# Kernel tuning notes

Measured on AMD Instinct MI355X. Metric: run time of the kernel, lower is better.

## Reference

```python
import jax, jax.numpy as jnp
import numpy as np

ROUTING_ITERS = 3


def squash(v):
    # v: [..., D]; l2norm over last dim
    l2 = jnp.linalg.norm(v, axis=-1, keepdims=True)
    unit = v / l2
    factor = (l2 * l2) / (1.0 + l2 * l2)
    return unit * factor


def setup_inputs() -> dict:
    key = jax.random.key(0)
    k1, k2 = jax.random.split(key)
    B, N_in, D_in = 256, 1152, 8
    N_out, D_out = 10, 16
    x = jax.random.normal(k1, (B, N_in, D_in), dtype=jnp.float32)
    W = jax.random.normal(k2, (N_in, N_out, D_out, D_in), dtype=jnp.float32)
    return {"x": x, "W": W}


def reference(x, W):
    # x: [B, N_in, D_in], W: [N_in, N_out, D_out, D_in]
    # u_hat[b,i,o,:] = W[i,o] @ x[b,i]
    u_hat = jnp.einsum('iodk,bik->biod', W, x)  # [B, N_in, N_out, D_out]
    N_in, N_out = W.shape[0], W.shape[1]
    b_logits = jnp.zeros((N_in, N_out), dtype=x.dtype)
    s = None
    for r in range(ROUTING_ITERS + 1):
        c = jax.nn.softmax(b_logits, axis=-1)            # [N_in, N_out]
        s = jnp.einsum('io,biod->bod', c, u_hat)          # [B, N_out, D_out]
        s = squash(s)
        if r < ROUTING_ITERS:
            # agreement summed over batch (matches original .sum(dim=0))
            b_logits = b_logits + jnp.einsum('biod,bod->io', u_hat, s)
    return s
```

## Files before the change

### kernel.cpp

```cpp
#include <hip/hip_runtime.h>
#include <math.h>

typedef __attribute__((ext_vector_type(8))) short bf16x8;
typedef __attribute__((ext_vector_type(4))) float f32x4;
typedef unsigned short u16;
typedef unsigned int u32;

#define NI    1152
#define DI    8
#define NO    10
#define DOUT  16
#define F     160
#define KTOT  9216
#define KS    288
#define SK    72

#define OFF_W2F 0
#define OFF_XFH 1474560
#define OFF_XFL 2654208
#define OFF_XTH 3833856
#define OFF_XTL 5013504
#define OFF_SFH 6193152
#define OFF_SFL 6213632
#define OFF_P   6234112
#define OFF_BA  9183232
#define OFF_BB  9194752
#define OFF_TP  9206272

union U8 { u16 u[8]; uint4 v; };

__device__ inline u16 bf16hi(float x) {
    u32 u = __float_as_uint(x);
    return (u16)((u + 0x7FFFu + ((u >> 16) & 1u)) >> 16);
}
__device__ inline float bf2f(u16 h) { return __uint_as_float(((u32)h) << 16); }

__global__ void prep(const float* __restrict__ x, const float* __restrict__ W,
                     float* __restrict__ W2f,
                     u16* __restrict__ xfh, u16* __restrict__ xfl,
                     u16* __restrict__ xth, u16* __restrict__ xtl,
                     float* __restrict__ blogA) {
    int u = blockIdx.x * 256 + threadIdx.x;
    if (u < 184320) {
        if (u < NI * NO) blogA[u] = 0.f;
        int ul = u & 63, tmp = u >> 6;
        int ks = tmp % KS, o = tmp / KS;
        int i = ks * 4 + (ul >> 4), d = ul & 15;
        const float* wp = W + ((size_t)(i * NO + o) * DOUT + d) * DI;
        float4 a = ((const float4*)wp)[0], b = ((const float4*)wp)[1];
        float* dst = W2f + (size_t)tmp * 512 + ul * 8;
        ((float4*)dst)[0] = a; ((float4*)dst)[1] = b;
    } else if (u < 479232) {
        int q = u - 184320;
        int ul = q & 63, tmp = q >> 6;
        int ks = tmp % KS, mt = tmp / KS;
        const float* xp = x + (size_t)(mt * 16 + (ul & 15)) * KTOT + ks * 32 + (ul >> 4) * 8;
        float4 a = ((const float4*)xp)[0], b = ((const float4*)xp)[1];
        float v[8] = {a.x, a.y, a.z, a.w, b.x, b.y, b.z, b.w};
        U8 ph, pl;
#pragma unroll
        for (int j = 0; j < 8; j++) {
            u16 h = bf16hi(v[j]);
            ph.u[j] = h; pl.u[j] = bf16hi(v[j] - bf2f(h));
        }
        *(uint4*)(xfh + (size_t)tmp * 512 + ul * 8) = ph.v;
        *(uint4*)(xfl + (size_t)tmp * 512 + ul * 8) = pl.v;
    } else if (u < 774144) {
        int q = u - 479232;
        int ul = q & 63, tmp = q >> 6;
        int ks8 = tmp & 7, ns = tmp >> 3;
        U8 ph, pl;
#pragma unroll
        for (int j = 0; j < 8; j++) {
            float v = x[(size_t)(ks8 * 32 + (ul >> 4) * 8 + j) * KTOT + ns * 16 + (ul & 15)];
            u16 h = bf16hi(v);
            ph.u[j] = h; pl.u[j] = bf16hi(v - bf2f(h));
        }
        *(uint4*)(xth + (size_t)tmp * 512 + ul * 8) = ph.v;
        *(uint4*)(xtl + (size_t)tmp * 512 + ul * 8) = pl.v;
    }
}

__global__ __launch_bounds__(256) void s_round(const u16* __restrict__ xfh,
                                               const u16* __restrict__ xfl,
                                               const float* __restrict__ W2f,
                                               const float* __restrict__ tpart,
                                               const float* __restrict__ blogIn,
                                               float* __restrict__ blogOut,
                                               float* __restrict__ P, int isR0) {
    __shared__ __attribute__((aligned(16))) u16 cwhS[10240];
    __shared__ __attribute__((aligned(16))) u16 cwlS[10240];
    __shared__ float ts[16][NO];
    __shared__ float cls[16][NO];

    const int t = threadIdx.x, l = t & 63, w = t >> 6;
    const int bid = blockIdx.x;
    const int sk  = bid % SK;
    const int fh  = (bid / SK) & 1;
    const int btg = bid / (2 * SK);

    if (isR0) {
        if (t < 160) cls[t / NO][t % NO] = 0.1f;
    } else {
        if (t < 160) {
            int il = t / NO, o = t % NO;
            int ig = sk * 16 + il;
            float a = tpart[(size_t)ig * NO + o] +
                      tpart[(size_t)(NI + ig) * NO + o] +
                      tpart[(size_t)(2 * NI + ig) * NO + o] +
                      tpart[(size_t)(3 * NI + ig) * NO + o];
            float bnew = blogIn[ig * NO + o] + a;
            blogOut[ig * NO + o] = bnew;
            ts[il][o] = bnew;
        }
        __syncthreads();
        if (t < 16) {
            float m = -3.402823466e+38f;
#pragma unroll
            for (int o = 0; o < NO; o++) m = fmaxf(m, ts[t][o]);
            float e[NO];
            float sum = 0.f;
#pragma unroll
            for (int o = 0; o < NO; o++) { e[o] = expf(ts[t][o] - m); sum += e[o]; }
            float inv = 1.f / sum;
#pragma unroll
            for (int o = 0; o < NO; o++) cls[t][o] = e[o] * inv;
        }
    }
    __syncthreads();

#pragma unroll
    for (int p = 0; p < 5; p++) {
        int vid  = p * 256 + t;
        int frag = vid >> 6;
        int ll   = vid & 63;
        int n = frag >> 2, kk = frag & 3;
        int ks = sk * 4 + kk;
        float cv = cls[kk * 4 + (ll >> 4)][fh * 5 + n];
        size_t base = ((size_t)((fh * 5 + n) * KS + ks)) * 512 + ll * 8;
        float4 a = ((const float4*)(W2f + base))[0];
        float4 b = ((const float4*)(W2f + base))[1];
        float v[8] = {a.x, a.y, a.z, a.w, b.x, b.y, b.z, b.w};
        U8 ph, pl;
#pragma unroll
        for (int j = 0; j < 8; j++) {
            float pv = cv * v[j];
            u16 h = bf16hi(pv);
            ph.u[j] = h; pl.u[j] = bf16hi(pv - bf2f(h));
        }
        *(uint4*)(cwhS + frag * 512 + ll * 8) = ph.v;
        *(uint4*)(cwlS + frag * 512 + ll * 8) = pl.v;
    }
    __syncthreads();

    const int bt = btg * 4 + w;
    f32x4 z = {0.f, 0.f, 0.f, 0.f};
    f32x4 acc[5];
#pragma unroll
    for (int n = 0; n < 5; n++) acc[n] = z;

#pragma unroll
    for (int kk = 0; kk < 4; kk++) {
        int ks = sk * 4 + kk;
        size_t ai = ((size_t)(bt * KS + ks)) * 512 + l * 8;
        bf16x8 ah = *(const bf16x8*)(xfh + ai);
        bf16x8 al = *(const bf16x8*)(xfl + ai);
#pragma unroll
        for (int n = 0; n < 5; n++) {
            bf16x8 bh = *(const bf16x8*)(cwhS + (n * 4 + kk) * 512 + l * 8);
            bf16x8 bl = *(const bf16x8*)(cwlS + (n * 4 + kk) * 512 + l * 8);
            acc[n] = __builtin_amdgcn_mfma_f32_16x16x32_bf16(ah, bh, acc[n], 0, 0, 0);
            acc[n] = __builtin_amdgcn_mfma_f32_16x16x32_bf16(ah, bl, acc[n], 0, 0, 0);
            acc[n] = __builtin_amdgcn_mfma_f32_16x16x32_bf16(al, bh, acc[n], 0, 0, 0);
        }
    }
    const int c0 = l & 15, rg = l >> 4;
    float* Pp = P + (size_t)sk * 40960 + (size_t)(bt * 16 + rg * 4) * F + fh * 80 + c0;
#pragma unroll
    for (int n = 0; n < 5; n++)
#pragma unroll
        for (int rr = 0; rr < 4; rr++)
            Pp[(size_t)rr * F + n * 16] = acc[n][rr];
}

__global__ void rs(const float* __restrict__ P, float* __restrict__ sout,
                   u16* __restrict__ sfh, u16* __restrict__ sfl) {
    int idx = blockIdx.x * 256 + threadIdx.x;
    float sum = 0.f;
#pragma unroll 8
    for (int sk2 = 0; sk2 < SK; sk2++) sum += P[(size_t)sk2 * 40960 + idx];
    float n2 = sum * sum;
#pragma unroll
    for (int off = 8; off > 0; off >>= 1) n2 += __shfl_xor(n2, off, 16);
    float l2v = sqrtf(n2);
    float scale = l2v / (1.f + n2);
    float sv = sum * scale;
    sout[idx] = sv;
    int b = idx / F, f = idx % F;
    size_t si = (size_t)((f >> 4) * 8 + (b >> 5)) * 512 +
                (size_t)(((b >> 3) & 3) * 16 + (f & 15)) * 8 + (b & 7);
    u16 h = bf16hi(sv);
    sfh[si] = h;
    sfl[si] = bf16hi(sv - bf2f(h));
}

__global__ __launch_bounds__(256) void c1(const u16* __restrict__ sfh,
                                          const u16* __restrict__ sfl,
                                          const u16* __restrict__ xth,
                                          const u16* __restrict__ xtl,
                                          const float* __restrict__ W,
                                          float* __restrict__ tpart) {
    __shared__ __attribute__((aligned(16))) float G[160 * 68];
    const int t = threadIdx.x, l = t & 63, w = t >> 6;
    const int nb = blockIdx.x >> 2, bq = blockIdx.x & 3;
    const int wm = w & 1, wn = w >> 1;

    f32x4 z = {0.f, 0.f, 0.f, 0.f};
    f32x4 acc[5][2];
#pragma unroll
    for (int m = 0; m < 5; m++)
#pragma unroll
        for (int n = 0; n < 2; n++) acc[m][n] = z;

#pragma unroll
    for (int ksl = 0; ksl < 2; ksl++) {
        int ksb = bq * 2 + ksl;
        bf16x8 ah[5], al[5];
#pragma unroll
        for (int m = 0; m < 5; m++) {
            size_t ai = ((size_t)((wm * 5 + m) * 8 + ksb)) * 512 + l * 8;
            ah[m] = *(const bf16x8*)(sfh + ai);
            al[m] = *(const bf16x8*)(sfl + ai);
        }
#pragma unroll
        for (int nl = 0; nl < 2; nl++) {
            size_t bi = ((size_t)((nb * 4 + wn * 2 + nl) * 8 + ksb)) * 512 + l * 8;
            bf16x8 bh = *(const bf16x8*)(xth + bi);
            bf16x8 blo = *(const bf16x8*)(xtl + bi);
#pragma unroll
            for (int m = 0; m < 5; m++) {
                acc[m][nl] = __builtin_amdgcn_mfma_f32_16x16x32_bf16(ah[m], bh, acc[m][nl], 0, 0, 0);
                acc[m][nl] = __builtin_amdgcn_mfma_f32_16x16x32_bf16(ah[m], blo, acc[m][nl], 0, 0, 0);
                acc[m][nl] = __builtin_amdgcn_mfma_f32_16x16x32_bf16(al[m], bh, acc[m][nl], 0, 0, 0);
            }
        }
    }
    const int c0 = l & 15, rg = l >> 4;
#pragma unroll
    for (int m = 0; m < 5; m++)
#pragma unroll
        for (int nl = 0; nl < 2; nl++)
#pragma unroll
            for (int rr = 0; rr < 4; rr++)
                G[(wm * 80 + m * 16 + rg * 4 + rr) * 68 + wn * 32 + nl * 16 + c0] = acc[m][nl][rr];
    __syncthreads();
    if (t < 160) {
        int i_l = t / 20, o = (t % 20) >> 1, dh = t & 1;
        int i_g = nb * 8 + i_l;
        const float* wp = W + (size_t)(i_g * NO + o) * 128 + dh * 64;
        float sum = 0.f;
#pragma unroll
        for (int d = 0; d < 8; d++) {
            const float* gp = &G[(o * 16 + dh * 8 + d) * 68 + i_l * 8];
            float4 g0 = ((const float4*)gp)[0], g1 = ((const float4*)gp)[1];
            float4 w0 = ((const float4*)(wp + d * 8))[0], w1 = ((const float4*)(wp + d * 8))[1];
            sum += g0.x * w0.x + g0.y * w0.y + g0.z * w0.z + g0.w * w0.w +
                   g1.x * w1.x + g1.y * w1.y + g1.z * w1.z + g1.w * w1.w;
        }
        sum += __shfl_xor(sum, 1);
        if (dh == 0) tpart[(size_t)(bq * NI + i_g) * NO + o] = sum;
    }
}

extern "C" void kernel_launch(void* const* d_in, const int* in_sizes, int n_in,
                              void* d_out, int out_size, void* d_ws, size_t ws_size,
                              hipStream_t stream) {
    const float* x = (const float*)d_in[0];
    const float* W = (const float*)d_in[1];
    float* out = (float*)d_out;
    float* ws  = (float*)d_ws;
    float* W2f = ws + OFF_W2F;
    u16* xfh = (u16*)(ws + OFF_XFH);
    u16* xfl = (u16*)(ws + OFF_XFL);
    u16* xth = (u16*)(ws + OFF_XTH);
    u16* xtl = (u16*)(ws + OFF_XTL);
    u16* sfh = (u16*)(ws + OFF_SFH);
    u16* sfl = (u16*)(ws + OFF_SFL);
    float* P   = ws + OFF_P;
    float* blA = ws + OFF_BA;
    float* blB = ws + OFF_BB;
    float* tp  = ws + OFF_TP;

    prep<<<3024, 256, 0, stream>>>(x, W, W2f, xfh, xfl, xth, xtl, blA);

    for (int r = 0; r < 4; r++) {
        const float* bIn = (r == 2) ? blB : blA;
        float* bOut      = (r == 2) ? blA : blB;
        s_round<<<576, 256, 0, stream>>>(xfh, xfl, W2f, tp, bIn, bOut, P, r == 0 ? 1 : 0);
        rs<<<160, 256, 0, stream>>>(P, out, sfh, sfl);
        if (r < 3)
            c1<<<576, 256, 0, stream>>>(sfh, sfl, xth, xtl, W, tp);
    }
}
```

Before: 100.1 us.

## Fuse routing s-round and squash reduction into one kernel per round

Replaces the split-K s_round kernel and the separate rs reduction with one sq_round kernel. Each 1024-thread block owns one 16-batch tile and one output capsule, and its 16 waves split K and reduce through shared memory before squashing. This removes the large partial-sum buffer P, its write and read traffic, and one launch per round. Routing logits now accumulate in place in c1 through taccum (+=), and each block recomputes softmax over all inputs, which replaces the logit ping-pong buffers. The cost is only 160 blocks instead of 576, plus much more repeated L2 reading of W2f and x across blocks.

```diff
diff --git a/kernel.cpp b/kernel.cpp
--- a/kernel.cpp
+++ b/kernel.cpp
@@ -13,7 +13,6 @@
 #define F     160
 #define KTOT  9216
 #define KS    288
-#define SK    72
 
 #define OFF_W2F 0
 #define OFF_XFH 1474560
@@ -22,12 +21,9 @@
 #define OFF_XTL 5013504
 #define OFF_SFH 6193152
 #define OFF_SFL 6213632
-#define OFF_P   6234112
-#define OFF_BA  9183232
-#define OFF_BB  9194752
-#define OFF_TP  9206272
-
-union U8 { u16 u[8]; uint4 v; };
+#define OFF_TP  6234112
+
+union U8 { u16 u[8]; uint4 v; bf16x8 b; };
 
 __device__ inline u16 bf16hi(float x) {
     u32 u = __float_as_uint(x);
@@ -39,10 +35,10 @@
                      float* __restrict__ W2f,
                      u16* __restrict__ xfh, u16* __restrict__ xfl,
                      u16* __restrict__ xth, u16* __restrict__ xtl,
-                     float* __restrict__ blogA) {
+                     float* __restrict__ taccum) {
     int u = blockIdx.x * 256 + threadIdx.x;
     if (u < 184320) {
-        if (u < NI * NO) blogA[u] = 0.f;
+        if (u < 4 * NI * NO) taccum[u] = 0.f;
         int ul = u & 63, tmp = u >> 6;
         int ks = tmp % KS, o = tmp / KS;
         int i = ks * 4 + (ul >> 4), d = ul & 15;
@@ -81,127 +77,88 @@
     }
 }
 
-__global__ __launch_bounds__(256) void s_round(const u16* __restrict__ xfh,
-                                               const u16* __restrict__ xfl,
-                                               const float* __restrict__ W2f,
-                                               const float* __restrict__ tpart,
-                                               const float* __restrict__ blogIn,
-                                               float* __restrict__ blogOut,
-                                               float* __restrict__ P, int isR0) {
-    __shared__ __attribute__((aligned(16))) u16 cwhS[10240];
-    __shared__ __attribute__((aligned(16))) u16 cwlS[10240];
-    __shared__ float ts[16][NO];
-    __shared__ float cls[16][NO];
+__global__ __launch_bounds__(1024) void sq_round(const u16* __restrict__ xfh,
+                                                 const u16* __restrict__ xfl,
+                                                 const float* __restrict__ W2f,
+                                                 const float* __restrict__ taccum,
+                                                 u16* __restrict__ sfh,
+                                                 u16* __restrict__ sfl,
+                                                 float* __restrict__ out, int r) {
+    __shared__ float cls[NI];
+    __shared__ __attribute__((aligned(16))) float Pl[16 * 256];
 
     const int t = threadIdx.x, l = t & 63, w = t >> 6;
-    const int bid = blockIdx.x;
-    const int sk  = bid % SK;
-    const int fh  = (bid / SK) & 1;
-    const int btg = bid / (2 * SK);
-
-    if (isR0) {
-        if (t < 160) cls[t / NO][t % NO] = 0.1f;
-    } else {
-        if (t < 160) {
-            int il = t / NO, o = t % NO;
-            int ig = sk * 16 + il;
-            float a = tpart[(size_t)ig * NO + o] +
-                      tpart[(size_t)(NI + ig) * NO + o] +
-                      tpart[(size_t)(2 * NI + ig) * NO + o] +
-                      tpart[(size_t)(3 * NI + ig) * NO + o];
-            float bnew = blogIn[ig * NO + o] + a;
-            blogOut[ig * NO + o] = bnew;
-            ts[il][o] = bnew;
-        }
-        __syncthreads();
-        if (t < 16) {
-            float m = -3.402823466e+38f;
-#pragma unroll
-            for (int o = 0; o < NO; o++) m = fmaxf(m, ts[t][o]);
-            float e[NO];
-            float sum = 0.f;
-#pragma unroll
-            for (int o = 0; o < NO; o++) { e[o] = expf(ts[t][o] - m); sum += e[o]; }
-            float inv = 1.f / sum;
-#pragma unroll
-            for (int o = 0; o < NO; o++) cls[t][o] = e[o] * inv;
-        }
+    const int btg = blockIdx.x;
+    const int o   = blockIdx.y;
+
+    for (int i = t; i < NI; i += 1024) {
+        float bv[NO];
+        float m = -3.402823466e+38f;
+#pragma unroll
+        for (int oo = 0; oo < NO; oo++) {
+            float a = taccum[i * NO + oo] + taccum[(NI + i) * NO + oo] +
+                      taccum[(2 * NI + i) * NO + oo] + taccum[(3 * NI + i) * NO + oo];
+            bv[oo] = a;
+            m = fmaxf(m, a);
+        }
+        float sum = 0.f;
+#pragma unroll
+        for (int oo = 0; oo < NO; oo++) { bv[oo] = expf(bv[oo] - m); sum += bv[oo]; }
+        cls[i] = bv[o] * (1.f / sum);
     }
     __syncthreads();
 
-#pragma unroll
-    for (int p = 0; p < 5; p++) {
-        int vid  = p * 256 + t;
-        int frag = vid >> 6;
-        int ll   = vid & 63;
-        int n = frag >> 2, kk = frag & 3;
-        int ks = sk * 4 + kk;
-        float cv = cls[kk * 4 + (ll >> 4)][fh * 5 + n];
-        size_t base = ((size_t)((fh * 5 + n) * KS + ks)) * 512 + ll * 8;
-        float4 a = ((const float4*)(W2f + base))[0];
-        float4 b = ((const float4*)(W2f + base))[1];
-        float v[8] = {a.x, a.y, a.z, a.w, b.x, b.y, b.z, b.w};
-        U8 ph, pl;
-#pragma unroll
-        for (int j = 0; j < 8; j++) {
-            float pv = cv * v[j];
-            u16 h = bf16hi(pv);
-            ph.u[j] = h; pl.u[j] = bf16hi(pv - bf2f(h));
-        }
-        *(uint4*)(cwhS + frag * 512 + ll * 8) = ph.v;
-        *(uint4*)(cwlS + frag * 512 + ll * 8) = pl.v;
-    }
-    __syncthreads();
-
-    const int bt = btg * 4 + w;
-    f32x4 z = {0.f, 0.f, 0.f, 0.f};
-    f32x4 acc[5];
-#pragma unroll
-    for (int n = 0; n < 5; n++) acc[n] = z;
-
-#pragma unroll
-    for (int kk = 0; kk < 4; kk++) {
-        int ks = sk * 4 + kk;
-        size_t ai = ((size_t)(bt * KS + ks)) * 512 + l * 8;
+    f32x4 acc = {0.f, 0.f, 0.f, 0.f};
+    const int ks0 = w * 18;
+#pragma unroll 3
+    for (int kk = 0; kk < 18; kk++) {
+        int ks = ks0 + kk;
+        size_t ai = ((size_t)(btg * KS + ks)) * 512 + l * 8;
         bf16x8 ah = *(const bf16x8*)(xfh + ai);
         bf16x8 al = *(const bf16x8*)(xfl + ai);
-#pragma unroll
-        for (int n = 0; n < 5; n++) {
-            bf16x8 bh = *(const bf16x8*)(cwhS + (n * 4 + kk) * 512 + l * 8);
-            bf16x8 bl = *(const bf16x8*)(cwlS + (n * 4 + kk) * 512 + l * 8);
-            acc[n] = __builtin_amdgcn_mfma_f32_16x16x32_bf16(ah, bh, acc[n], 0, 0, 0);
-            acc[n] = __builtin_amdgcn_mfma_f32_16x16x32_bf16(ah, bl, acc[n], 0, 0, 0);
-            acc[n] = __builtin_amdgcn_mfma_f32_16x16x32_bf16(al, bh, acc[n], 0, 0, 0);
-        }
+        float cv = cls[ks * 4 + (l >> 4)];
+        const float* wp = W2f + ((size_t)(o * KS + ks)) * 512 + l * 8;
+        float4 a4 = ((const float4*)wp)[0];
+        float4 b4 = ((const float4*)wp)[1];
+        float v[8] = {a4.x, a4.y, a4.z, a4.w, b4.x, b4.y, b4.z, b4.w};
+        U8 ph, pl;
+#pragma unroll
+        for (int j = 0; j < 8; j++) {
+            float p = cv * v[j];
+            u16 h = bf16hi(p);
+            ph.u[j] = h; pl.u[j] = bf16hi(p - bf2f(h));
+        }
+        acc = __builtin_amdgcn_mfma_f32_16x16x32_bf16(ah, ph.b, acc, 0, 0, 0);
+        acc = __builtin_amdgcn_mfma_f32_16x16x32_bf16(ah, pl.b, acc, 0, 0, 0);
+        acc = __builtin_amdgcn_mfma_f32_16x16x32_bf16(al, ph.b, acc, 0, 0, 0);
     }
     const int c0 = l & 15, rg = l >> 4;
-    float* Pp = P + (size_t)sk * 40960 + (size_t)(bt * 16 + rg * 4) * F + fh * 80 + c0;
-#pragma unroll
-    for (int n = 0; n < 5; n++)
-#pragma unroll
-        for (int rr = 0; rr < 4; rr++)
-            Pp[(size_t)rr * F + n * 16] = acc[n][rr];
-}
-
-__global__ void rs(const float* __restrict__ P, float* __restrict__ sout,
-                   u16* __restrict__ sfh, u16* __restrict__ sfl) {
-    int idx = blockIdx.x * 256 + threadIdx.x;
-    float sum = 0.f;
-#pragma unroll 8
-    for (int sk2 = 0; sk2 < SK; sk2++) sum += P[(size_t)sk2 * 40960 + idx];
-    float n2 = sum * sum;
-#pragma unroll
-    for (int off = 8; off > 0; off >>= 1) n2 += __shfl_xor(n2, off, 16);
-    float l2v = sqrtf(n2);
-    float scale = l2v / (1.f + n2);
-    float sv = sum * scale;
-    sout[idx] = sv;
-    int b = idx / F, f = idx % F;
-    size_t si = (size_t)((f >> 4) * 8 + (b >> 5)) * 512 +
-                (size_t)(((b >> 3) & 3) * 16 + (f & 15)) * 8 + (b & 7);
-    u16 h = bf16hi(sv);
-    sfh[si] = h;
-    sfl[si] = bf16hi(sv - bf2f(h));
+#pragma unroll
+    for (int rr = 0; rr < 4; rr++)
+        Pl[w * 256 + (rg * 4 + rr) * 16 + c0] = acc[rr];
+    __syncthreads();
+
+    if (t < 256) {
+        float sum = 0.f;
+#pragma unroll
+        for (int ww = 0; ww < 16; ww++) sum += Pl[ww * 256 + t];
+        float n2 = sum * sum;
+#pragma unroll
+        for (int off = 8; off > 0; off >>= 1) n2 += __shfl_xor(n2, off, 16);
+        float l2v = sqrtf(n2);
+        float scale = l2v / (1.f + n2);
+        float sv = sum * scale;
+        int b = btg * 16 + (t >> 4), d = t & 15;
+        if (r == 3) {
+            out[b * F + o * 16 + d] = sv;
+        } else {
+            size_t si = (size_t)(o * 8 + (b >> 5)) * 512 +
+                        (size_t)(((b >> 3) & 3) * 16 + d) * 8 + (b & 7);
+            u16 h = bf16hi(sv);
+            sfh[si] = h;
+            sfl[si] = bf16hi(sv - bf2f(h));
+        }
+    }
 }
 
 __global__ __launch_bounds__(256) void c1(const u16* __restrict__ sfh,
@@ -209,7 +166,7 @@
                                           const u16* __restrict__ xth,
                                           const u16* __restrict__ xtl,
                                           const float* __restrict__ W,
-                                          float* __restrict__ tpart) {
+                                          float* __restrict__ taccum) {
     __shared__ __attribute__((aligned(16))) float G[160 * 68];
     const int t = threadIdx.x, l = t & 63, w = t >> 6;
     const int nb = blockIdx.x >> 2, bq = blockIdx.x & 3;
@@ -268,7 +225,7 @@
                    g1.x * w1.x + g1.y * w1.y + g1.z * w1.z + g1.w * w1.w;
         }
         sum += __shfl_xor(sum, 1);
-        if (dh == 0) tpart[(size_t)(bq * NI + i_g) * NO + o] = sum;
+        if (dh == 0) taccum[(size_t)(bq * NI + i_g) * NO + o] += sum;
     }
 }
 
@@ -286,18 +243,12 @@
     u16* xtl = (u16*)(ws + OFF_XTL);
     u16* sfh = (u16*)(ws + OFF_SFH);
     u16* sfl = (u16*)(ws + OFF_SFL);
-    float* P   = ws + OFF_P;
-    float* blA = ws + OFF_BA;
-    float* blB = ws + OFF_BB;
-    float* tp  = ws + OFF_TP;
-
-    prep<<<3024, 256, 0, stream>>>(x, W, W2f, xfh, xfl, xth, xtl, blA);
+    float* tp = ws + OFF_TP;
+
+    prep<<<3024, 256, 0, stream>>>(x, W, W2f, xfh, xfl, xth, xtl, tp);
 
     for (int r = 0; r < 4; r++) {
-        const float* bIn = (r == 2) ? blB : blA;
-        float* bOut      = (r == 2) ? blA : blB;
-        s_round<<<576, 256, 0, stream>>>(xfh, xfl, W2f, tp, bIn, bOut, P, r == 0 ? 1 : 0);
-        rs<<<160, 256, 0, stream>>>(P, out, sfh, sfl);
+        sq_round<<<dim3(16, 10), 1024, 0, stream>>>(xfh, xfl, W2f, tp, sfh, sfl, out, r);
         if (r < 3)
             c1<<<576, 256, 0, stream>>>(sfh, sfl, xth, xtl, W, tp);
     }
```

Result: slower. 119.4 us (+19.3%).

## Remove prep kernel; convert x and W to split-bf16 on the fly in consumers

Applied to the files above, without the earlier changes.

Drops the preprocessing kernel that wrote reordered W and hi/lo bf16 copies of x and x-transposed. s_round now reads x and W in fp32 straight from the inputs and splits them into bf16 hi/lo in registers. c1 gathers strided columns of x and splits them the same way. The blog buffer is no longer zeroed; round 1 uses zero instead of reading it. This removes one launch and several MB of workspace writes, at the cost of repeated conversion work and uncoalesced strided x reads in c1 on every round.

```diff
diff --git a/kernel.cpp b/kernel.cpp
--- a/kernel.cpp
+++ b/kernel.cpp
@@ -15,19 +15,14 @@
 #define KS    288
 #define SK    72
 
-#define OFF_W2F 0
-#define OFF_XFH 1474560
-#define OFF_XFL 2654208
-#define OFF_XTH 3833856
-#define OFF_XTL 5013504
-#define OFF_SFH 6193152
-#define OFF_SFL 6213632
-#define OFF_P   6234112
-#define OFF_BA  9183232
-#define OFF_BB  9194752
-#define OFF_TP  9206272
-
-union U8 { u16 u[8]; uint4 v; };
+#define OFF_SFH 0
+#define OFF_SFL 20480
+#define OFF_P   40960
+#define OFF_BA  2990080
+#define OFF_BB  3001600
+#define OFF_TP  3013120
+
+union U8 { u16 u[8]; uint4 v; bf16x8 b; };
 
 __device__ inline u16 bf16hi(float x) {
     u32 u = __float_as_uint(x);
@@ -35,59 +30,23 @@
 }
 __device__ inline float bf2f(u16 h) { return __uint_as_float(((u32)h) << 16); }
 
-__global__ void prep(const float* __restrict__ x, const float* __restrict__ W,
-                     float* __restrict__ W2f,
-                     u16* __restrict__ xfh, u16* __restrict__ xfl,
-                     u16* __restrict__ xth, u16* __restrict__ xtl,
-                     float* __restrict__ blogA) {
-    int u = blockIdx.x * 256 + threadIdx.x;
-    if (u < 184320) {
-        if (u < NI * NO) blogA[u] = 0.f;
-        int ul = u & 63, tmp = u >> 6;
-        int ks = tmp % KS, o = tmp / KS;
-        int i = ks * 4 + (ul >> 4), d = ul & 15;
-        const float* wp = W + ((size_t)(i * NO + o) * DOUT + d) * DI;
-        float4 a = ((const float4*)wp)[0], b = ((const float4*)wp)[1];
-        float* dst = W2f + (size_t)tmp * 512 + ul * 8;
-        ((float4*)dst)[0] = a; ((float4*)dst)[1] = b;
-    } else if (u < 479232) {
-        int q = u - 184320;
-        int ul = q & 63, tmp = q >> 6;
-        int ks = tmp % KS, mt = tmp / KS;
-        const float* xp = x + (size_t)(mt * 16 + (ul & 15)) * KTOT + ks * 32 + (ul >> 4) * 8;
-        float4 a = ((const float4*)xp)[0], b = ((const float4*)xp)[1];
-        float v[8] = {a.x, a.y, a.z, a.w, b.x, b.y, b.z, b.w};
-        U8 ph, pl;
-#pragma unroll
-        for (int j = 0; j < 8; j++) {
-            u16 h = bf16hi(v[j]);
-            ph.u[j] = h; pl.u[j] = bf16hi(v[j] - bf2f(h));
-        }
-        *(uint4*)(xfh + (size_t)tmp * 512 + ul * 8) = ph.v;
-        *(uint4*)(xfl + (size_t)tmp * 512 + ul * 8) = pl.v;
-    } else if (u < 774144) {
-        int q = u - 479232;
-        int ul = q & 63, tmp = q >> 6;
-        int ks8 = tmp & 7, ns = tmp >> 3;
-        U8 ph, pl;
-#pragma unroll
-        for (int j = 0; j < 8; j++) {
-            float v = x[(size_t)(ks8 * 32 + (ul >> 4) * 8 + j) * KTOT + ns * 16 + (ul & 15)];
-            u16 h = bf16hi(v);
-            ph.u[j] = h; pl.u[j] = bf16hi(v - bf2f(h));
-        }
-        *(uint4*)(xth + (size_t)tmp * 512 + ul * 8) = ph.v;
-        *(uint4*)(xtl + (size_t)tmp * 512 + ul * 8) = pl.v;
-    }
-}
-
-__global__ __launch_bounds__(256) void s_round(const u16* __restrict__ xfh,
-                                               const u16* __restrict__ xfl,
-                                               const float* __restrict__ W2f,
+__device__ inline void split8(const float* v, bf16x8* bh, bf16x8* bl) {
+    U8 h, l;
+#pragma unroll
+    for (int j = 0; j < 8; j++) {
+        u16 hh = bf16hi(v[j]);
+        h.u[j] = hh;
+        l.u[j] = bf16hi(v[j] - bf2f(hh));
+    }
+    *bh = h.b; *bl = l.b;
+}
+
+__global__ __launch_bounds__(256) void s_round(const float* __restrict__ x,
+                                               const float* __restrict__ W,
                                                const float* __restrict__ tpart,
                                                const float* __restrict__ blogIn,
                                                float* __restrict__ blogOut,
-                                               float* __restrict__ P, int isR0) {
+                                               float* __restrict__ P, int mode) {
     __shared__ __attribute__((aligned(16))) u16 cwhS[10240];
     __shared__ __attribute__((aligned(16))) u16 cwlS[10240];
     __shared__ float ts[16][NO];
@@ -99,7 +58,7 @@
     const int fh  = (bid / SK) & 1;
     const int btg = bid / (2 * SK);
 
-    if (isR0) {
+    if (mode == 0) {
         if (t < 160) cls[t / NO][t % NO] = 0.1f;
     } else {
         if (t < 160) {
@@ -109,7 +68,7 @@
                       tpart[(size_t)(NI + ig) * NO + o] +
                       tpart[(size_t)(2 * NI + ig) * NO + o] +
                       tpart[(size_t)(3 * NI + ig) * NO + o];
-            float bnew = blogIn[ig * NO + o] + a;
+            float bnew = (mode == 2 ? blogIn[ig * NO + o] : 0.f) + a;
             blogOut[ig * NO + o] = bnew;
             ts[il][o] = bnew;
         }
@@ -136,17 +95,18 @@
         int ll   = vid & 63;
         int n = frag >> 2, kk = frag & 3;
         int ks = sk * 4 + kk;
-        float cv = cls[kk * 4 + (ll >> 4)][fh * 5 + n];
-        size_t base = ((size_t)((fh * 5 + n) * KS + ks)) * 512 + ll * 8;
-        float4 a = ((const float4*)(W2f + base))[0];
-        float4 b = ((const float4*)(W2f + base))[1];
-        float v[8] = {a.x, a.y, a.z, a.w, b.x, b.y, b.z, b.w};
+        int o  = fh * 5 + n;
+        int i  = ks * 4 + (ll >> 4), d = ll & 15;
+        float cv = cls[kk * 4 + (ll >> 4)][o];
+        const float* wp = W + ((size_t)(i * NO + o) * DOUT + d) * DI;
+        float4 a = ((const float4*)wp)[0];
+        float4 b = ((const float4*)wp)[1];
+        float v[8] = {cv*a.x, cv*a.y, cv*a.z, cv*a.w, cv*b.x, cv*b.y, cv*b.z, cv*b.w};
         U8 ph, pl;
 #pragma unroll
         for (int j = 0; j < 8; j++) {
-            float pv = cv * v[j];
-            u16 h = bf16hi(pv);
-            ph.u[j] = h; pl.u[j] = bf16hi(pv - bf2f(h));
+            u16 h = bf16hi(v[j]);
+            ph.u[j] = h; pl.u[j] = bf16hi(v[j] - bf2f(h));
         }
         *(uint4*)(cwhS + frag * 512 + ll * 8) = ph.v;
         *(uint4*)(cwlS + frag * 512 + ll * 8) = pl.v;
@@ -162,9 +122,12 @@
 #pragma unroll
     for (int kk = 0; kk < 4; kk++) {
         int ks = sk * 4 + kk;
-        size_t ai = ((size_t)(bt * KS + ks)) * 512 + l * 8;
-        bf16x8 ah = *(const bf16x8*)(xfh + ai);
-        bf16x8 al = *(const bf16x8*)(xfl + ai);
+        const float* xp = x + (size_t)(bt * 16 + (l & 15)) * KTOT + ks * 32 + (l >> 4) * 8;
+        float4 a4 = ((const float4*)xp)[0];
+        float4 b4 = ((const float4*)xp)[1];
+        float v[8] = {a4.x, a4.y, a4.z, a4.w, b4.x, b4.y, b4.z, b4.w};
+        bf16x8 ah, al;
+        split8(v, &ah, &al);
 #pragma unroll
         for (int n = 0; n < 5; n++) {
             bf16x8 bh = *(const bf16x8*)(cwhS + (n * 4 + kk) * 512 + l * 8);
@@ -184,7 +147,7 @@
 }
 
 __global__ void rs(const float* __restrict__ P, float* __restrict__ sout,
-                   u16* __restrict__ sfh, u16* __restrict__ sfl) {
+                   u16* __restrict__ sfh, u16* __restrict__ sfl, int last) {
     int idx = blockIdx.x * 256 + threadIdx.x;
     float sum = 0.f;
 #pragma unroll 8
@@ -195,19 +158,21 @@
     float l2v = sqrtf(n2);
     float scale = l2v / (1.f + n2);
     float sv = sum * scale;
-    sout[idx] = sv;
-    int b = idx / F, f = idx % F;
-    size_t si = (size_t)((f >> 4) * 8 + (b >> 5)) * 512 +
-                (size_t)(((b >> 3) & 3) * 16 + (f & 15)) * 8 + (b & 7);
-    u16 h = bf16hi(sv);
-    sfh[si] = h;
-    sfl[si] = bf16hi(sv - bf2f(h));
+    if (last) {
+        sout[idx] = sv;
+    } else {
+        int b = idx / F, f = idx % F;
+        size_t si = (size_t)((f >> 4) * 8 + (b >> 5)) * 512 +
+                    (size_t)(((b >> 3) & 3) * 16 + (f & 15)) * 8 + (b & 7);
+        u16 h = bf16hi(sv);
+        sfh[si] = h;
+        sfl[si] = bf16hi(sv - bf2f(h));
+    }
 }
 
 __global__ __launch_bounds__(256) void c1(const u16* __restrict__ sfh,
                                           const u16* __restrict__ sfl,
-                                          const u16* __restrict__ xth,
-                                          const u16* __restrict__ xtl,
+                                          const float* __restrict__ x,
                                           const float* __restrict__ W,
                                           float* __restrict__ tpart) {
     __shared__ __attribute__((aligned(16))) float G[160 * 68];
@@ -234,9 +199,13 @@
         }
 #pragma unroll
         for (int nl = 0; nl < 2; nl++) {
-            size_t bi = ((size_t)((nb * 4 + wn * 2 + nl) * 8 + ksb)) * 512 + l * 8;
-            bf16x8 bh = *(const bf16x8*)(xth + bi);
-            bf16x8 blo = *(const bf16x8*)(xtl + bi);
+            int ns = nb * 4 + wn * 2 + nl;
+            const float* xp = x + (size_t)(ksb * 32 + (l >> 4) * 8) * KTOT + ns * 16 + (l & 15);
+            float v[8];
+#pragma unroll
+            for (int j = 0; j < 8; j++) v[j] = xp[(size_t)j * KTOT];
+            bf16x8 bh, blo;
+            split8(v, &bh, &blo);
 #pragma unroll
             for (int m = 0; m < 5; m++) {
                 acc[m][nl] = __builtin_amdgcn_mfma_f32_16x16x32_bf16(ah[m], bh, acc[m][nl], 0, 0, 0);
@@ -279,11 +248,6 @@
     const float* W = (const float*)d_in[1];
     float* out = (float*)d_out;
     float* ws  = (float*)d_ws;
-    float* W2f = ws + OFF_W2F;
-    u16* xfh = (u16*)(ws + OFF_XFH);
-    u16* xfl = (u16*)(ws + OFF_XFL);
-    u16* xth = (u16*)(ws + OFF_XTH);
-    u16* xtl = (u16*)(ws + OFF_XTL);
     u16* sfh = (u16*)(ws + OFF_SFH);
     u16* sfl = (u16*)(ws + OFF_SFL);
     float* P   = ws + OFF_P;
@@ -291,14 +255,13 @@
     float* blB = ws + OFF_BB;
     float* tp  = ws + OFF_TP;
 
-    prep<<<3024, 256, 0, stream>>>(x, W, W2f, xfh, xfl, xth, xtl, blA);
-
     for (int r = 0; r < 4; r++) {
+        int mode = (r == 0) ? 0 : (r == 1 ? 1 : 2);
         const float* bIn = (r == 2) ? blB : blA;
         float* bOut      = (r == 2) ? blA : blB;
-        s_round<<<576, 256, 0, stream>>>(xfh, xfl, W2f, tp, bIn, bOut, P, r == 0 ? 1 : 0);
-        rs<<<160, 256, 0, stream>>>(P, out, sfh, sfl);
+        s_round<<<576, 256, 0, stream>>>(x, W, tp, bIn, bOut, P, mode);
+        rs<<<160, 256, 0, stream>>>(P, out, sfh, sfl, r == 3 ? 1 : 0);
         if (r < 3)
-            c1<<<576, 256, 0, stream>>>(sfh, sfl, xth, xtl, W, tp);
-    }
-}
+            c1<<<576, 256, 0, stream>>>(sfh, sfl, x, W, tp);
+    }
+}
```

Result: no change. 98.33 us (median of 2 runs) (-1.7%).
